# Kernel tuning notes

Measured on AMD Instinct MI355X. Metric: run time of the kernel, lower is better.

## Reference

```python
import jax, jax.numpy as jnp
import numpy as np

BS, CIN, COUT, OUT_DIM, S, S0 = 64, 128, 128, 1024, 2, 1
BLK = S * (S0 + 1)  # 4
D = OUT_DIM * BLK   # 4096


def setup_inputs() -> dict:
    key = jax.random.key(0)
    kx, kw = jax.random.split(key)
    x = jax.random.normal(kx, (BS, CIN, D), dtype=jnp.float32)
    weight = jax.random.normal(kw, (COUT, CIN, D), dtype=jnp.float32)
    return {"x": x, "weight": weight}


def reference(x, weight):
    # Equivalent to: (x[:, None] * weight).reshape(bs, cout, cin, out_dim, blk).sum((-1, -3)) / sqrt(cin)
    bs, cin, d = x.shape
    cout = weight.shape[0]
    blk = BLK
    xr = x.reshape(bs, cin, d // blk, blk)          # (bs, cin, out_dim, blk)
    wr = weight.reshape(cout, cin, d // blk, blk)   # (cout, cin, out_dim, blk)
    # Blocked locally-connected contraction over (cin, blk), fused -- never
    # materializes the (bs, cout, cin, d) broadcast intermediate.
    out = jnp.einsum('bink,oink->bon', xr, wr)
    return out / jnp.sqrt(jnp.asarray(cin, dtype=x.dtype))
```

## Files before the change

kernel.cpp:

```cpp
#include <hip/hip_runtime.h>


#define BSZ    64
#define CIN    128
#define COUT   128
#define ODIM   1024
#define DDIM   4096
#define NB     4
#define CI     8
#define NCHUNK (CIN/CI)
#define LROW   40
#define PX     (64*LROW + 8)
#define PW     (128*LROW + 8)

typedef short  bf16x8 __attribute__((ext_vector_type(8)));
typedef short  s16x4  __attribute__((ext_vector_type(4)));
typedef float  f32x4  __attribute__((ext_vector_type(4)));

static __device__ __forceinline__ unsigned short f2bf(float f) {
    unsigned int u = __float_as_uint(f);
    u += 0x7fffu + ((u >> 16) & 1u);
    return (unsigned short)(u >> 16);
}

__global__ __launch_bounds__(1024, 4)
void nolc_kernel(const float* __restrict__ xg,
                 const float* __restrict__ wg,
                 float* __restrict__ outg) {
    __shared__ short xs[NB * PX];
    __shared__ short ws[NB * PW];

    const int bid = blockIdx.x;
    const int bn  = (bid & 7) * 32 + (bid >> 3);
    const int t    = threadIdx.x;
    const int lane = t & 63;
    const int wave = t >> 6;

    const int dbase = 16 * bn;

    const int bt = wave & 3;
    const int oq = wave >> 2;
    const int row = lane & 15;
    const int kg  = lane >> 4;

    f32x4 acc[2][4];
#pragma unroll
    for (int j = 0; j < 2; ++j)
#pragma unroll
        for (int n = 0; n < 4; ++n)
            acc[j][n] = (f32x4){0.f, 0.f, 0.f, 0.f};

    for (int c = 0; c < NCHUNK; ++c) {
        const int i0 = c * CI;

#pragma unroll
        for (int it = 0; it < 2; ++it) {
            int L  = it * 1024 + t;
            int n  = L & 3;
            int ii = (L >> 2) & 7;
            int b  = L >> 5;
            const float4 v = *reinterpret_cast<const float4*>(
                xg + (size_t)(b * CIN + i0 + ii) * DDIM + dbase + 4 * n);
            s16x4 s;
            s[0] = (short)f2bf(v.x); s[1] = (short)f2bf(v.y);
            s[2] = (short)f2bf(v.z); s[3] = (short)f2bf(v.w);
            *reinterpret_cast<s16x4*>(&xs[n * PX + b * LROW + ii * 4]) = s;
        }
#pragma unroll
        for (int it = 0; it < 4; ++it) {
            int L  = it * 1024 + t;
            int n  = L & 3;
            int ii = (L >> 2) & 7;
            int o  = L >> 5;
            const float4 v = *reinterpret_cast<const float4*>(
                wg + (size_t)(o * CIN + i0 + ii) * DDIM + dbase + 4 * n);
            s16x4 s;
            s[0] = (short)f2bf(v.x); s[1] = (short)f2bf(v.y);
            s[2] = (short)f2bf(v.z); s[3] = (short)f2bf(v.w);
            *reinterpret_cast<s16x4*>(&ws[n * PW + o * LROW + ii * 4]) = s;
        }
        __syncthreads();

        const short* xb = &xs[(bt * 16 + row) * LROW + kg * 8];
        const short* wb = &ws[(oq * 32 + row) * LROW + kg * 8];
#pragma unroll
        for (int n = 0; n < 4; ++n) {
            bf16x8 a = *reinterpret_cast<const bf16x8*>(xb + n * PX);
#pragma unroll
            for (int j = 0; j < 2; ++j) {
                bf16x8 bb = *reinterpret_cast<const bf16x8*>(wb + n * PW + j * 16 * LROW);
                acc[j][n] = __builtin_amdgcn_mfma_f32_16x16x32_bf16(a, bb, acc[j][n], 0, 0, 0);
            }
        }
        __syncthreads();
    }

    const float scale = 0.08838834764831845f;
#pragma unroll
    for (int j = 0; j < 2; ++j) {
        const int o = oq * 32 + j * 16 + row;
#pragma unroll
        for (int r = 0; r < 4; ++r) {
            const int b = bt * 16 + kg * 4 + r;
            float4 v;
            v.x = acc[j][0][r] * scale;
            v.y = acc[j][1][r] * scale;
            v.z = acc[j][2][r] * scale;
            v.w = acc[j][3][r] * scale;
            *reinterpret_cast<float4*>(
                outg + ((size_t)b * COUT + o) * ODIM + 4 * bn) = v;
        }
    }
}

extern "C" void kernel_launch(void* const* d_in, const int* in_sizes, int n_in,
                              void* d_out, int out_size, void* d_ws, size_t ws_size,
                              hipStream_t stream) {
    const float* x = (const float*)d_in[0];
    const float* w = (const float*)d_in[1];
    float* out = (float*)d_out;
    nolc_kernel<<<dim3(256), dim3(1024), 0, stream>>>(x, w, out);
}
```

Before: 143.0 us.

## Split output channels across blocks and double-buffer LDS with register prefetch

Each block now covers half of the output channels, giving 512 blocks of 512 threads instead of 256 blocks of 1024. The K-chunk loop is software-pipelined: the next chunk's global loads go into registers while the current chunk is converted and staged into one of two LDS buffers. The second __syncthreads per chunk becomes a single s_barrier. The aim is to hide global-load latency behind MFMA work and raise parallelism. The cost is that each x tile is now read twice (once per output half), plus extra register pressure.

New measurement: 163.6 us. +14.4%, slower.

```diff
diff --git a/kernel.cpp b/kernel.cpp
--- a/kernel.cpp
+++ b/kernel.cpp
@@ -1,7 +1,6 @@
 #include <hip/hip_runtime.h>
 
 
-#define BSZ    64
 #define CIN    128
 #define COUT   128
 #define ODIM   1024
@@ -9,9 +8,9 @@
 #define NB     4
 #define CI     8
 #define NCHUNK (CIN/CI)
-#define LROW   40
-#define PX     (64*LROW + 8)
-#define PW     (128*LROW + 8)
+#define LROW   36
+#define XPL    (64*LROW + 2)
+#define BUFS   (NB*XPL)
 
 typedef short  bf16x8 __attribute__((ext_vector_type(8)));
 typedef short  s16x4  __attribute__((ext_vector_type(4)));
@@ -22,24 +21,43 @@
     u += 0x7fffu + ((u >> 16) & 1u);
     return (unsigned short)(u >> 16);
 }
+static __device__ __forceinline__ s16x4 cvt4(float4 v) {
+    s16x4 s;
+    s[0] = (short)f2bf(v.x); s[1] = (short)f2bf(v.y);
+    s[2] = (short)f2bf(v.z); s[3] = (short)f2bf(v.w);
+    return s;
+}
 
-__global__ __launch_bounds__(1024, 4)
+__global__ __launch_bounds__(512, 4)
 void nolc_kernel(const float* __restrict__ xg,
                  const float* __restrict__ wg,
                  float* __restrict__ outg) {
-    __shared__ short xs[NB * PX];
-    __shared__ short ws[NB * PW];
+    __shared__ short xs[2 * BUFS];
+    __shared__ short ws[2 * BUFS];
 
-    const int bid = blockIdx.x;
-    const int bn  = (bid & 7) * 32 + (bid >> 3);
+    const int bid  = blockIdx.x;
+    const int xcd  = bid & 7;
+    const int gidx = xcd * 64 + (bid >> 3);
+    const int bn   = gidx >> 1;
+    const int oh   = gidx & 1;
+
     const int t    = threadIdx.x;
     const int lane = t & 63;
     const int wave = t >> 6;
-
     const int dbase = 16 * bn;
 
-    const int bt = wave & 3;
-    const int oq = wave >> 2;
+    const int sn  = t & 3;
+    const int sii = (t >> 2) & 7;
+    const int sr  = t >> 5;
+    const size_t ITS  = (size_t)16 * CIN * DDIM;
+    const size_t CSTR = (size_t)CI * DDIM;
+
+    const float* xp = xg + (size_t)(sr * CIN + sii) * DDIM + dbase + 4 * sn;
+    const float* wp = wg + ((size_t)(oh * 64 + sr) * CIN + sii) * DDIM + dbase + 4 * sn;
+    const int ldso = sn * XPL + sr * LROW + sii * 4;
+
+    const int bt  = wave & 3;
+    const int ot  = wave >> 2;
     const int row = lane & 15;
     const int kg  = lane >> 4;
 
@@ -50,55 +68,65 @@
         for (int n = 0; n < 4; ++n)
             acc[j][n] = (f32x4){0.f, 0.f, 0.f, 0.f};
 
-    for (int c = 0; c < NCHUNK; ++c) {
-        const int i0 = c * CI;
+    float4 rxA[4], rwA[4], rxB[4], rwB[4];
 
-#pragma unroll
-        for (int it = 0; it < 2; ++it) {
-            int L  = it * 1024 + t;
-            int n  = L & 3;
-            int ii = (L >> 2) & 7;
-            int b  = L >> 5;
-            const float4 v = *reinterpret_cast<const float4*>(
-                xg + (size_t)(b * CIN + i0 + ii) * DDIM + dbase + 4 * n);
-            s16x4 s;
-            s[0] = (short)f2bf(v.x); s[1] = (short)f2bf(v.y);
-            s[2] = (short)f2bf(v.z); s[3] = (short)f2bf(v.w);
-            *reinterpret_cast<s16x4*>(&xs[n * PX + b * LROW + ii * 4]) = s;
-        }
-#pragma unroll
-        for (int it = 0; it < 4; ++it) {
-            int L  = it * 1024 + t;
-            int n  = L & 3;
-            int ii = (L >> 2) & 7;
-            int o  = L >> 5;
-            const float4 v = *reinterpret_cast<const float4*>(
-                wg + (size_t)(o * CIN + i0 + ii) * DDIM + dbase + 4 * n);
-            s16x4 s;
-            s[0] = (short)f2bf(v.x); s[1] = (short)f2bf(v.y);
-            s[2] = (short)f2bf(v.z); s[3] = (short)f2bf(v.w);
-            *reinterpret_cast<s16x4*>(&ws[n * PW + o * LROW + ii * 4]) = s;
-        }
-        __syncthreads();
+#define LOADC(rx, rw, c)                                                     \
+    do {                                                                     \
+        const float* _xp = xp + (size_t)(c) * CSTR;                          \
+        const float* _wp = wp + (size_t)(c) * CSTR;                          \
+        _Pragma("unroll")                                                    \
+        for (int it = 0; it < 4; ++it) {                                     \
+            rx[it] = *reinterpret_cast<const float4*>(_xp + it * ITS);       \
+            rw[it] = *reinterpret_cast<const float4*>(_wp + it * ITS);       \
+        }                                                                    \
+    } while (0)
 
-        const short* xb = &xs[(bt * 16 + row) * LROW + kg * 8];
-        const short* wb = &ws[(oq * 32 + row) * LROW + kg * 8];
-#pragma unroll
-        for (int n = 0; n < 4; ++n) {
-            bf16x8 a = *reinterpret_cast<const bf16x8*>(xb + n * PX);
-#pragma unroll
-            for (int j = 0; j < 2; ++j) {
-                bf16x8 bb = *reinterpret_cast<const bf16x8*>(wb + n * PW + j * 16 * LROW);
-                acc[j][n] = __builtin_amdgcn_mfma_f32_16x16x32_bf16(a, bb, acc[j][n], 0, 0, 0);
-            }
-        }
-        __syncthreads();
+#define STAGE(rx, rw, sel)                                                   \
+    do {                                                                     \
+        _Pragma("unroll")                                                    \
+        for (int it = 0; it < 4; ++it) {                                     \
+            *reinterpret_cast<s16x4*>(&xs[(sel) * BUFS + ldso + it * 16 * LROW]) = cvt4(rx[it]); \
+            *reinterpret_cast<s16x4*>(&ws[(sel) * BUFS + ldso + it * 16 * LROW]) = cvt4(rw[it]); \
+        }                                                                    \
+    } while (0)
+
+#define COMPUTE(sel)                                                         \
+    do {                                                                     \
+        const short* _xb = &xs[(sel) * BUFS + (bt * 16 + row) * LROW + kg * 8]; \
+        const short* _wb = &ws[(sel) * BUFS + (ot * 32 + row) * LROW + kg * 8]; \
+        _Pragma("unroll")                                                    \
+        for (int n = 0; n < 4; ++n) {                                        \
+            bf16x8 a = *reinterpret_cast<const bf16x8*>(_xb + n * XPL);      \
+            _Pragma("unroll")                                                \
+            for (int j = 0; j < 2; ++j) {                                    \
+                bf16x8 bb = *reinterpret_cast<const bf16x8*>(_wb + n * XPL + j * 16 * LROW); \
+                acc[j][n] = __builtin_amdgcn_mfma_f32_16x16x32_bf16(a, bb, acc[j][n], 0, 0, 0); \
+            }                                                                \
+        }                                                                    \
+    } while (0)
+
+    LOADC(rxA, rwA, 0);
+    for (int c = 0; c < NCHUNK; c += 2) {
+        LOADC(rxB, rwB, c + 1);
+        STAGE(rxA, rwA, 0);
+        asm volatile("s_waitcnt lgkmcnt(0)" ::: "memory");
+        __builtin_amdgcn_s_barrier();
+        COMPUTE(0);
+
+        if (c + 2 < NCHUNK) LOADC(rxA, rwA, c + 2);
+        STAGE(rxB, rwB, 1);
+        asm volatile("s_waitcnt lgkmcnt(0)" ::: "memory");
+        __builtin_amdgcn_s_barrier();
+        COMPUTE(1);
     }
+#undef LOADC
+#undef STAGE
+#undef COMPUTE
 
     const float scale = 0.08838834764831845f;
 #pragma unroll
     for (int j = 0; j < 2; ++j) {
-        const int o = oq * 32 + j * 16 + row;
+        const int o = oh * 64 + ot * 32 + j * 16 + row;
 #pragma unroll
         for (int r = 0; r < 4; ++r) {
             const int b = bt * 16 + kg * 4 + r;
@@ -107,8 +135,7 @@
             v.y = acc[j][1][r] * scale;
             v.z = acc[j][2][r] * scale;
             v.w = acc[j][3][r] * scale;
-            *reinterpret_cast<float4*>(
-                outg + ((size_t)b * COUT + o) * ODIM + 4 * bn) = v;
+            *reinterpret_cast<float4*>(outg + ((size_t)b * COUT + o) * ODIM + 4 * bn) = v;
         }
     }
 }
@@ -119,5 +146,5 @@
     const float* x = (const float*)d_in[0];
     const float* w = (const float*)d_in[1];
     float* out = (float*)d_out;
-    nolc_kernel<<<dim3(256), dim3(1024), 0, stream>>>(x, w, out);
+    nolc_kernel<<<dim3(512), dim3(512), 0, stream>>>(x, w, out);
 }
```

## Load MFMA fragments directly from global memory, dropping LDS staging and barriers

Applied to the files above, without the earlier changes.

Replaces the shared-memory staging of bf16-converted x and weight tiles with direct per-lane global loads that form MFMA fragments in registers. The grid is repartitioned into 512 blocks of 256 threads, each covering half the batch for a 16-column d slice. Each wave now computes a 2x2 tile of 16x16 outputs per d group. This removes the LDS round trip and the __syncthreads barriers. The cost is that weight data is read from global twice, once per batch half, and the per-lane loads are strided and less coalesced.

New measurement: 344.2 us. 141% more time.

```diff
diff --git a/kernel.cpp b/kernel.cpp
--- a/kernel.cpp
+++ b/kernel.cpp
@@ -1,116 +1,117 @@
 #include <hip/hip_runtime.h>
 
 
-#define BSZ    64
-#define CIN    128
-#define COUT   128
-#define ODIM   1024
-#define DDIM   4096
-#define NB     4
-#define CI     8
-#define NCHUNK (CIN/CI)
-#define LROW   40
-#define PX     (64*LROW + 8)
-#define PW     (128*LROW + 8)
+#define CIN  128
+#define COUT 128
+#define ODIM 1024
+#define DDIM 4096
 
-typedef short  bf16x8 __attribute__((ext_vector_type(8)));
-typedef short  s16x4  __attribute__((ext_vector_type(4)));
-typedef float  f32x4  __attribute__((ext_vector_type(4)));
+typedef short bf16x8 __attribute__((ext_vector_type(8)));
+typedef float f32x4  __attribute__((ext_vector_type(4)));
 
 static __device__ __forceinline__ unsigned short f2bf(float f) {
     unsigned int u = __float_as_uint(f);
     u += 0x7fffu + ((u >> 16) & 1u);
     return (unsigned short)(u >> 16);
 }
+static __device__ __forceinline__ bf16x8 mkfrag(float4 a, float4 b) {
+    bf16x8 r;
+    r[0] = (short)f2bf(a.x); r[1] = (short)f2bf(a.y);
+    r[2] = (short)f2bf(a.z); r[3] = (short)f2bf(a.w);
+    r[4] = (short)f2bf(b.x); r[5] = (short)f2bf(b.y);
+    r[6] = (short)f2bf(b.z); r[7] = (short)f2bf(b.w);
+    return r;
+}
 
-__global__ __launch_bounds__(1024, 4)
+__global__ __launch_bounds__(256, 2)
 void nolc_kernel(const float* __restrict__ xg,
                  const float* __restrict__ wg,
                  float* __restrict__ outg) {
-    __shared__ short xs[NB * PX];
-    __shared__ short ws[NB * PW];
+    const int bid  = blockIdx.x;
+    const int gidx = (bid & 7) * 64 + (bid >> 3);
+    const int bq   = (gidx >> 1) & 1;
+    const int ng   = (gidx >> 2) * 2 + (gidx & 1);
 
-    const int bid = blockIdx.x;
-    const int bn  = (bid & 7) * 32 + (bid >> 3);
-    const int t    = threadIdx.x;
-    const int lane = t & 63;
-    const int wave = t >> 6;
+    const int lane = threadIdx.x & 63;
+    const int oq   = threadIdx.x >> 6;
+    const int row  = lane & 15;
+    const int kg   = lane >> 4;
 
-    const int dbase = 16 * bn;
+    const int d0 = ng * 16;
 
-    const int bt = wave & 3;
-    const int oq = wave >> 2;
-    const int row = lane & 15;
-    const int kg  = lane >> 4;
+    const float* xr0 = xg + ((size_t)(bq * 32 + row) * CIN + kg * 2) * DDIM + d0;
+    const float* xr1 = xr0 + (size_t)16 * CIN * DDIM;
+    const float* wr0 = wg + ((size_t)(oq * 32 + row) * CIN + kg * 2) * DDIM + d0;
+    const float* wr1 = wr0 + (size_t)16 * CIN * DDIM;
 
-    f32x4 acc[2][4];
+    f32x4 acc[2][2][4];
 #pragma unroll
-    for (int j = 0; j < 2; ++j)
+    for (int bh = 0; bh < 2; ++bh)
 #pragma unroll
-        for (int n = 0; n < 4; ++n)
-            acc[j][n] = (f32x4){0.f, 0.f, 0.f, 0.f};
+        for (int oh = 0; oh < 2; ++oh)
+#pragma unroll
+            for (int nn = 0; nn < 4; ++nn)
+                acc[bh][oh][nn] = (f32x4){0.f, 0.f, 0.f, 0.f};
 
-    for (int c = 0; c < NCHUNK; ++c) {
-        const int i0 = c * CI;
+#pragma unroll 1
+    for (int kk = 0; kk < 16; ++kk) {
+        const size_t ko = (size_t)kk * 8 * DDIM;
+
+        float4 fa[2][4][2], fb[2][4][2];
+#pragma unroll
+        for (int nn = 0; nn < 4; ++nn)
+#pragma unroll
+            for (int j = 0; j < 2; ++j) {
+                fa[0][nn][j] = *reinterpret_cast<const float4*>(xr0 + ko + j * DDIM + nn * 4);
+                fa[1][nn][j] = *reinterpret_cast<const float4*>(xr1 + ko + j * DDIM + nn * 4);
+            }
+#pragma unroll
+        for (int nn = 0; nn < 4; ++nn)
+#pragma unroll
+            for (int j = 0; j < 2; ++j) {
+                fb[0][nn][j] = *reinterpret_cast<const float4*>(wr0 + ko + j * DDIM + nn * 4);
+                fb[1][nn][j] = *reinterpret_cast<const float4*>(wr1 + ko + j * DDIM + nn * 4);
+            }
+
+        bf16x8 A[2][4], B[2][4];
+#pragma unroll
+        for (int bh = 0; bh < 2; ++bh)
+#pragma unroll
+            for (int nn = 0; nn < 4; ++nn)
+                A[bh][nn] = mkfrag(fa[bh][nn][0], fa[bh][nn][1]);
+#pragma unroll
+        for (int oh = 0; oh < 2; ++oh)
+#pragma unroll
+            for (int nn = 0; nn < 4; ++nn)
+                B[oh][nn] = mkfrag(fb[oh][nn][0], fb[oh][nn][1]);
 
 #pragma unroll
-        for (int it = 0; it < 2; ++it) {
-            int L  = it * 1024 + t;
-            int n  = L & 3;
-            int ii = (L >> 2) & 7;
-            int b  = L >> 5;
-            const float4 v = *reinterpret_cast<const float4*>(
-                xg + (size_t)(b * CIN + i0 + ii) * DDIM + dbase + 4 * n);
-            s16x4 s;
-            s[0] = (short)f2bf(v.x); s[1] = (short)f2bf(v.y);
-            s[2] = (short)f2bf(v.z); s[3] = (short)f2bf(v.w);
-            *reinterpret_cast<s16x4*>(&xs[n * PX + b * LROW + ii * 4]) = s;
-        }
+        for (int nn = 0; nn < 4; ++nn)
 #pragma unroll
-        for (int it = 0; it < 4; ++it) {
-            int L  = it * 1024 + t;
-            int n  = L & 3;
-            int ii = (L >> 2) & 7;
-            int o  = L >> 5;
-            const float4 v = *reinterpret_cast<const float4*>(
-                wg + (size_t)(o * CIN + i0 + ii) * DDIM + dbase + 4 * n);
-            s16x4 s;
-            s[0] = (short)f2bf(v.x); s[1] = (short)f2bf(v.y);
-            s[2] = (short)f2bf(v.z); s[3] = (short)f2bf(v.w);
-            *reinterpret_cast<s16x4*>(&ws[n * PW + o * LROW + ii * 4]) = s;
-        }
-        __syncthreads();
-
-        const short* xb = &xs[(bt * 16 + row) * LROW + kg * 8];
-        const short* wb = &ws[(oq * 32 + row) * LROW + kg * 8];
+            for (int bh = 0; bh < 2; ++bh)
 #pragma unroll
-        for (int n = 0; n < 4; ++n) {
-            bf16x8 a = *reinterpret_cast<const bf16x8*>(xb + n * PX);
-#pragma unroll
-            for (int j = 0; j < 2; ++j) {
-                bf16x8 bb = *reinterpret_cast<const bf16x8*>(wb + n * PW + j * 16 * LROW);
-                acc[j][n] = __builtin_amdgcn_mfma_f32_16x16x32_bf16(a, bb, acc[j][n], 0, 0, 0);
-            }
-        }
-        __syncthreads();
+                for (int oh = 0; oh < 2; ++oh)
+                    acc[bh][oh][nn] = __builtin_amdgcn_mfma_f32_16x16x32_bf16(
+                        A[bh][nn], B[oh][nn], acc[bh][oh][nn], 0, 0, 0);
     }
 
     const float scale = 0.08838834764831845f;
 #pragma unroll
-    for (int j = 0; j < 2; ++j) {
-        const int o = oq * 32 + j * 16 + row;
+    for (int bh = 0; bh < 2; ++bh)
 #pragma unroll
-        for (int r = 0; r < 4; ++r) {
-            const int b = bt * 16 + kg * 4 + r;
-            float4 v;
-            v.x = acc[j][0][r] * scale;
-            v.y = acc[j][1][r] * scale;
-            v.z = acc[j][2][r] * scale;
-            v.w = acc[j][3][r] * scale;
-            *reinterpret_cast<float4*>(
-                outg + ((size_t)b * COUT + o) * ODIM + 4 * bn) = v;
+        for (int oh = 0; oh < 2; ++oh) {
+            const int o = oq * 32 + oh * 16 + row;
+#pragma unroll
+            for (int r = 0; r < 4; ++r) {
+                const int b = bq * 32 + bh * 16 + kg * 4 + r;
+                float4 v;
+                v.x = acc[bh][oh][0][r] * scale;
+                v.y = acc[bh][oh][1][r] * scale;
+                v.z = acc[bh][oh][2][r] * scale;
+                v.w = acc[bh][oh][3][r] * scale;
+                *reinterpret_cast<float4*>(outg + ((size_t)b * COUT + o) * ODIM + ng * 4) = v;
+            }
         }
-    }
 }
 
 extern "C" void kernel_launch(void* const* d_in, const int* in_sizes, int n_in,
@@ -119,5 +120,5 @@
     const float* x = (const float*)d_in[0];
     const float* w = (const float*)d_in[1];
     float* out = (float*)d_out;
-    nolc_kernel<<<dim3(256), dim3(1024), 0, stream>>>(x, w, out);
+    nolc_kernel<<<dim3(512), dim3(256), 0, stream>>>(x, w, out);
 }
```
